# Kernel optimization log

Hardware: AMD Instinct MI355X
Metric: run time of the kernel (lower is better)

## Reference

```python
import jax, jax.numpy as jnp
import numpy as np

N, M, D = 16384, 16384, 256

def setup_inputs() -> dict:
    key = jax.random.key(0)
    kx, ky, kp = jax.random.split(key, 3)
    x = jax.random.normal(kx, (N, D), dtype=jnp.float32)
    y = jax.random.normal(ky, (M, D), dtype=jnp.float32)
    psi = jax.random.normal(kp, (M,), dtype=jnp.float32)
    return {"x": x, "y": y, "psi": psi}

def reference(x, y, psi):
    # cxy[i,j] = ||x_i||^2 + ||y_j||^2 - 2 <x_i, y_j>   (squared euclidean)
    x2 = jnp.sum(x * x, axis=1, keepdims=True)          # [N,1]
    y2 = jnp.sum(y * y, axis=1)[None, :]                # [1,M]
    cxy = x2 + y2 - 2.0 * (x @ y.T)                     # [N,M]
    psi_conjugate_mean = jnp.mean(jnp.min(cxy - psi[None, :], axis=1))
    psi_mean = jnp.mean(psi)
    return (psi_conjugate_mean, psi_mean)
```

## Files before the change

kernel.cpp:

```cpp
#include <hip/hip_runtime.h>
#include <hip/hip_bf16.h>
#include <hip/hip_fp8.h>

#define N_ROWS 16384
#define M_ROWS 16384
#define DIM 256
#define JT 64
#define NJ 32

typedef __attribute__((ext_vector_type(4))) float f32x4;
typedef __attribute__((ext_vector_type(4))) int   i32x4;
typedef __attribute__((ext_vector_type(8))) int   i32x8;

__device__ inline unsigned enc_f(float f) {
  unsigned u = __float_as_uint(f);
  return (u & 0x80000000u) ? ~u : (u | 0x80000000u);
}
__device__ inline float dec_f(unsigned u) {
  unsigned b = (u & 0x80000000u) ? (u & 0x7FFFFFFFu) : ~u;
  return __uint_as_float(b);
}

__global__ __launch_bounds__(256) void prep_kernel(
    const float* __restrict__ x, const float* __restrict__ y,
    const float* __restrict__ psi,
    unsigned char* __restrict__ xb8, unsigned char* __restrict__ yb8,
    float* __restrict__ x2, float* __restrict__ rj,
    unsigned int* __restrict__ rowmin) {
  int bid  = blockIdx.x;
  int isY  = bid >= (N_ROWS / 4);
  int rb   = isY ? bid - N_ROWS / 4 : bid;
  int row  = rb * 4 + (threadIdx.x >> 6);
  int lane = threadIdx.x & 63;
  const float* in = isY ? y : x;
  unsigned char* outb = isY ? yb8 : xb8;
  const float4 v = *reinterpret_cast<const float4*>(in + (size_t)row * DIM + lane * 4);
  unsigned b0 = __hip_fp8_e4m3(v.x).__x;
  unsigned b1 = __hip_fp8_e4m3(v.y).__x;
  unsigned b2 = __hip_fp8_e4m3(v.z).__x;
  unsigned b3 = __hip_fp8_e4m3(v.w).__x;
  *reinterpret_cast<unsigned int*>(outb + (size_t)row * DIM + lane * 4) =
      b0 | (b1 << 8) | (b2 << 16) | (b3 << 24);
  float s = v.x * v.x + v.y * v.y + v.z * v.z + v.w * v.w;
#pragma unroll
  for (int m = 1; m < 64; m <<= 1) s += __shfl_xor(s, m, 64);
  if (lane == 0) {
    if (isY) rj[row] = s - psi[row];
    else { x2[row] = s; rowmin[row] = 0xFFFFFFFFu; }
  }
}

__global__ __launch_bounds__(256, 2) void gemm_min_kernel(
    const unsigned char* __restrict__ xb8, const unsigned char* __restrict__ yb8,
    const float* __restrict__ rj, unsigned int* __restrict__ rowmin) {
  __shared__ unsigned char Bt[3][JT * DIM];

  const int bid    = blockIdx.x;
  const int jchunk = bid & 7;
  const int strip  = bid >> 3;
  const int brow   = strip * 256;
  const int jbase0 = jchunk * (JT * NJ);

  const int tid = threadIdx.x;
  const int w = tid >> 6, lane = tid & 63;
  const int fr = lane & 15, g4 = lane >> 4;

  const int SC1 = 0x7F7F7F7F;

  i32x8 afr[4][2];
  {
    const unsigned char* aBase = xb8 + (size_t)(brow + w * 64 + fr) * DIM + g4 * 32;
#pragma unroll
    for (int m = 0; m < 4; ++m)
#pragma unroll
      for (int kq = 0; kq < 2; ++kq) {
        afr[m][kq] = *reinterpret_cast<const i32x8*>(aBase + (size_t)(m * 16) * DIM + kq * 128);
        asm volatile("" : "+a"(afr[m][kq]));
      }
  }
  __builtin_amdgcn_sched_barrier(0);

  const int sr16 = lane & 15;
  const int sk32 = (lane >> 4) * 32;

#define STAGE(buf, j)                                                            \
  {                                                                              \
    _Pragma("unroll")                                                            \
    for (int c = 0; c < 4; ++c) {                                                \
      const int p = w * 4 + c;                                                   \
      const int cc = p >> 1, h = p & 1;                                          \
      __builtin_amdgcn_global_load_lds(                                          \
          (const __attribute__((address_space(1))) void*)(                       \
              yb8 + (size_t)(jbase0 + (j) * JT + (cc >> 1) * 16 + sr16) * DIM +  \
              (cc & 1) * 128 + sk32 + h * 16),                                   \
          (__attribute__((address_space(3))) void*)(&Bt[(buf)][cc * 2048 + h * 1024]), \
          16, 0, 0);                                                             \
    }                                                                            \
  }

#define LOADF(dst, NG, KQ)                                                       \
  {                                                                              \
    const int cc = (NG) * 2 + (KQ);                                              \
    i32x4 lo = *reinterpret_cast<const i32x4*>(&B[cc * 2048 + lane * 16]);       \
    i32x4 hi = *reinterpret_cast<const i32x4*>(&B[cc * 2048 + 1024 + lane * 16]); \
    dst[0] = lo[0]; dst[1] = lo[1]; dst[2] = lo[2]; dst[3] = lo[3];              \
    dst[4] = hi[0]; dst[5] = hi[1]; dst[6] = hi[2]; dst[7] = hi[3];              \
  }

#define MFMA4(KQ, NG, PB)                                                        \
  {                                                                              \
    _Pragma("unroll")                                                            \
    for (int m = 0; m < 4; ++m)                                                  \
      acc[m][(NG)] = __builtin_amdgcn_mfma_scale_f32_16x16x128_f8f6f4(           \
          afr[m][(KQ)], PB, acc[m][(NG)], 0, 0, 0, SC1, 0, SC1);                 \
  }

#define SGB_DS_MFMA                                                              \
  __builtin_amdgcn_sched_group_barrier(0x100, 2, 0);                             \
  __builtin_amdgcn_sched_group_barrier(0x008, 4, 0);

  STAGE(0, 0);
  STAGE(1, 1);

  const float* rjc = rj + jbase0;
  float mn[4][4];
#pragma unroll
  for (int m = 0; m < 4; ++m)
#pragma unroll
    for (int r = 0; r < 4; ++r) mn[m][r] = 3.4e38f;

  int rb = 0;
#pragma unroll 1
  for (int j = 0; j < NJ; ++j) {
    if (j == NJ - 1) { asm volatile("s_waitcnt vmcnt(0)" ::: "memory"); }
    else             { asm volatile("s_waitcnt vmcnt(4)" ::: "memory"); }
    __builtin_amdgcn_sched_barrier(0);
    __builtin_amdgcn_s_barrier();
    __builtin_amdgcn_sched_barrier(0);

    float rv[4];
#pragma unroll
    for (int n = 0; n < 4; ++n) rv[n] = rjc[j * JT + n * 16 + fr];
    __builtin_amdgcn_sched_barrier(0);
    if (j + 2 < NJ) {
      int sb = rb + 2; if (sb >= 3) sb -= 3;
      STAGE(sb, j + 2);
    }
    __builtin_amdgcn_sched_barrier(0);

    f32x4 acc[4][4];
#pragma unroll
    for (int m = 0; m < 4; ++m)
#pragma unroll
      for (int n = 0; n < 4; ++n) acc[m][n] = (f32x4){0.f, 0.f, 0.f, 0.f};

    const unsigned char* B = &Bt[rb][0];
    i32x8 pbA, pbB;
    LOADF(pbA, 0, 0);

    __builtin_amdgcn_s_setprio(1);
    __builtin_amdgcn_sched_barrier(0);
    LOADF(pbB, 1, 0); MFMA4(0, 0, pbA); SGB_DS_MFMA;
    LOADF(pbA, 2, 0); MFMA4(0, 1, pbB); SGB_DS_MFMA;
    LOADF(pbB, 3, 0); MFMA4(0, 2, pbA); SGB_DS_MFMA;
    LOADF(pbA, 0, 1); MFMA4(0, 3, pbB); SGB_DS_MFMA;
    LOADF(pbB, 1, 1); MFMA4(1, 0, pbA); SGB_DS_MFMA;
    LOADF(pbA, 2, 1); MFMA4(1, 1, pbB); SGB_DS_MFMA;
    LOADF(pbB, 3, 1); MFMA4(1, 2, pbA); SGB_DS_MFMA;
    MFMA4(1, 3, pbB);
    __builtin_amdgcn_sched_group_barrier(0x008, 4, 0);
    __builtin_amdgcn_sched_barrier(0);
    __builtin_amdgcn_s_setprio(0);

#pragma unroll
    for (int m = 0; m < 4; ++m)
#pragma unroll
      for (int n = 0; n < 4; ++n)
#pragma unroll
        for (int r = 0; r < 4; ++r)
          mn[m][r] = fminf(mn[m][r], fmaf(-2.f, acc[m][n][r], rv[n]));
    rb = rb + 1; if (rb >= 3) rb -= 3;
  }
#undef SGB_DS_MFMA
#undef MFMA4
#undef LOADF
#undef STAGE

#pragma unroll
  for (int m = 0; m < 4; ++m)
#pragma unroll
    for (int r = 0; r < 4; ++r) {
      float v = mn[m][r];
#pragma unroll
      for (int s = 1; s < 16; s <<= 1) v = fminf(v, __shfl_xor(v, s, 64));
      if (fr == 0) {
        int row = brow + w * 64 + m * 16 + g4 * 4 + r;
        atomicMin(&rowmin[row], enc_f(v));
      }
    }
}

__global__ __launch_bounds__(256) void finish1_kernel(
    const float* __restrict__ x2, const unsigned int* __restrict__ rowmin,
    const float* __restrict__ psi, double* __restrict__ partials) {
  int tid = threadIdx.x;
  int i = blockIdx.x * 256 + tid;
  double s0 = (double)x2[i] + (double)dec_f(rowmin[i]);
  double s1 = (double)psi[i];
  __shared__ double sm0[4], sm1[4];
#pragma unroll
  for (int m = 1; m < 64; m <<= 1) { s0 += __shfl_xor(s0, m, 64); s1 += __shfl_xor(s1, m, 64); }
  if ((tid & 63) == 0) { sm0[tid >> 6] = s0; sm1[tid >> 6] = s1; }
  __syncthreads();
  if (tid == 0) {
    partials[blockIdx.x]      = sm0[0] + sm0[1] + sm0[2] + sm0[3];
    partials[64 + blockIdx.x] = sm1[0] + sm1[1] + sm1[2] + sm1[3];
  }
}

__global__ __launch_bounds__(64) void finish2_kernel(
    const double* __restrict__ partials, float* __restrict__ out) {
  int lane = threadIdx.x;
  double s0 = partials[lane];
  double s1 = partials[64 + lane];
#pragma unroll
  for (int m = 1; m < 64; m <<= 1) { s0 += __shfl_xor(s0, m, 64); s1 += __shfl_xor(s1, m, 64); }
  if (lane == 0) {
    out[0] = (float)(s0 / (double)N_ROWS);
    out[1] = (float)(s1 / (double)M_ROWS);
  }
}

extern "C" void kernel_launch(void* const* d_in, const int* in_sizes, int n_in,
                              void* d_out, int out_size, void* d_ws, size_t ws_size,
                              hipStream_t stream) {
  const float* x   = (const float*)d_in[0];
  const float* y   = (const float*)d_in[1];
  const float* psi = (const float*)d_in[2];
  float* out = (float*)d_out;

  char* ws = (char*)d_ws;
  unsigned char* xb8 = (unsigned char*)ws;
  unsigned char* yb8 = (unsigned char*)(ws + (size_t)N_ROWS * DIM);
  float* x2 = (float*)(ws + (size_t)(N_ROWS + M_ROWS) * DIM);
  float* rj = x2 + N_ROWS;
  unsigned int* rowmin = (unsigned int*)(rj + M_ROWS);
  double* partials = (double*)(rowmin + N_ROWS);

  prep_kernel<<<(N_ROWS + M_ROWS) / 4, 256, 0, stream>>>(x, y, psi, xb8, yb8, x2, rj, rowmin);
  gemm_min_kernel<<<(N_ROWS / 256) * 8, 256, 0, stream>>>(xb8, yb8, rj, rowmin);
  finish1_kernel<<<N_ROWS / 256, 256, 0, stream>>>(x2, rowmin, psi, partials);
  finish2_kernel<<<1, 64, 0, stream>>>(partials, out);
}
```

Baseline: 78.09 us.

## Double-buffer accumulators and fold the previous tile's max under current MFMAs

Splits the accumulator into two ping-pong sets so the min/fold epilogue of tile j-1 runs interleaved with the MFMAs of tile j, using sched_group_barrier to place VALU ops between matrix instructions. It also rewrites min(rv - 2*acc) as -2*max(acc - rv/2) by seeding the accumulators with -rv/2, which removes the per-element FMA and leaves only a max. The aim is to hide the VALU epilogue behind MFMA latency, at the cost of doubling accumulator registers (32 extra f32x4), which may lower occupancy or cause spills.

```diff
diff --git a/kernel.cpp b/kernel.cpp
--- a/kernel.cpp
+++ b/kernel.cpp
@@ -107,81 +107,99 @@
     dst[4] = hi[0]; dst[5] = hi[1]; dst[6] = hi[2]; dst[7] = hi[3];              \
   }
 
-#define MFMA4(KQ, NG, PB)                                                        \
+#define MFMA4(AC, KQ, NG, PB)                                                    \
   {                                                                              \
     _Pragma("unroll")                                                            \
     for (int m = 0; m < 4; ++m)                                                  \
-      acc[m][(NG)] = __builtin_amdgcn_mfma_scale_f32_16x16x128_f8f6f4(           \
-          afr[m][(KQ)], PB, acc[m][(NG)], 0, 0, 0, SC1, 0, SC1);                 \
-  }
-
-#define SGB_DS_MFMA                                                              \
+      AC[m][(NG)] = __builtin_amdgcn_mfma_scale_f32_16x16x128_f8f6f4(            \
+          afr[m][(KQ)], PB, AC[m][(NG)], 0, 0, 0, SC1, 0, SC1);                  \
+  }
+
+#define INIT16(AC, NG)                                                           \
+  {                                                                              \
+    _Pragma("unroll")                                                            \
+    for (int m = 0; m < 4; ++m)                                                  \
+      AC[m][(NG)] = (f32x4){nh[(NG)], nh[(NG)], nh[(NG)], nh[(NG)]};             \
+  }
+
+#define FOLD8(AP, G)                                                             \
+  {                                                                              \
+    _Pragma("unroll")                                                            \
+    for (int np = 0; np < 2; ++np)                                               \
+      _Pragma("unroll")                                                          \
+      for (int r = 0; r < 4; ++r)                                                \
+        mx[(G) >> 1][r] = fmaxf(mx[(G) >> 1][r],                                 \
+                                AP[(G) >> 1][((G) & 1) * 2 + np][r]);            \
+  }
+
+#define SGB_G                                                                    \
   __builtin_amdgcn_sched_group_barrier(0x100, 2, 0);                             \
-  __builtin_amdgcn_sched_group_barrier(0x008, 4, 0);
+  __builtin_amdgcn_sched_group_barrier(0x008, 4, 0);                             \
+  __builtin_amdgcn_sched_group_barrier(0x002, 24, 0);
+
+#define ITER(J, AC, AP)                                                          \
+  {                                                                              \
+    if ((J) == NJ - 1) { asm volatile("s_waitcnt vmcnt(0)" ::: "memory"); }      \
+    else               { asm volatile("s_waitcnt vmcnt(4)" ::: "memory"); }      \
+    __builtin_amdgcn_sched_barrier(0);                                           \
+    __builtin_amdgcn_s_barrier();                                                \
+    __builtin_amdgcn_sched_barrier(0);                                           \
+    float rv[4], nh[4];                                                          \
+    _Pragma("unroll")                                                            \
+    for (int n = 0; n < 4; ++n) rv[n] = rjc[(J) * JT + n * 16 + fr];             \
+    __builtin_amdgcn_sched_barrier(0);                                           \
+    if ((J) + 2 < NJ) { int sb = rb + 2; if (sb >= 3) sb -= 3; STAGE(sb, (J) + 2); } \
+    __builtin_amdgcn_sched_barrier(0);                                           \
+    _Pragma("unroll")                                                            \
+    for (int n = 0; n < 4; ++n) nh[n] = -0.5f * rv[n];                           \
+    const unsigned char* B = &Bt[rb][0];                                         \
+    i32x8 pbA, pbB;                                                              \
+    LOADF(pbA, 0, 0);                                                            \
+    __builtin_amdgcn_s_setprio(1);                                               \
+    __builtin_amdgcn_sched_barrier(0);                                           \
+    INIT16(AC, 0);                                                               \
+    LOADF(pbB, 1, 0); MFMA4(AC, 0, 0, pbA); INIT16(AC, 1); FOLD8(AP, 0); SGB_G;  \
+    LOADF(pbA, 2, 0); MFMA4(AC, 0, 1, pbB); INIT16(AC, 2); FOLD8(AP, 1); SGB_G;  \
+    LOADF(pbB, 3, 0); MFMA4(AC, 0, 2, pbA); INIT16(AC, 3); FOLD8(AP, 2); SGB_G;  \
+    LOADF(pbA, 0, 1); MFMA4(AC, 0, 3, pbB); FOLD8(AP, 3); SGB_G;                 \
+    LOADF(pbB, 1, 1); MFMA4(AC, 1, 0, pbA); FOLD8(AP, 4); SGB_G;                 \
+    LOADF(pbA, 2, 1); MFMA4(AC, 1, 1, pbB); FOLD8(AP, 5); SGB_G;                 \
+    LOADF(pbB, 3, 1); MFMA4(AC, 1, 2, pbA); FOLD8(AP, 6); SGB_G;                 \
+    MFMA4(AC, 1, 3, pbB); FOLD8(AP, 7);                                          \
+    __builtin_amdgcn_sched_group_barrier(0x008, 4, 0);                           \
+    __builtin_amdgcn_sched_group_barrier(0x002, 24, 0);                          \
+    __builtin_amdgcn_sched_barrier(0);                                           \
+    __builtin_amdgcn_s_setprio(0);                                               \
+    rb = rb + 1; if (rb >= 3) rb -= 3;                                           \
+  }
 
   STAGE(0, 0);
   STAGE(1, 1);
 
   const float* rjc = rj + jbase0;
-  float mn[4][4];
+  float mx[4][4];
+  f32x4 accA[4][4], accB[4][4];
 #pragma unroll
   for (int m = 0; m < 4; ++m)
 #pragma unroll
-    for (int r = 0; r < 4; ++r) mn[m][r] = 3.4e38f;
+    for (int r = 0; r < 4; ++r) mx[m][r] = -3.4e38f;
+#pragma unroll
+  for (int m = 0; m < 4; ++m)
+#pragma unroll
+    for (int n = 0; n < 4; ++n) accB[m][n] = (f32x4){-3.4e38f, -3.4e38f, -3.4e38f, -3.4e38f};
 
   int rb = 0;
 #pragma unroll 1
-  for (int j = 0; j < NJ; ++j) {
-    if (j == NJ - 1) { asm volatile("s_waitcnt vmcnt(0)" ::: "memory"); }
-    else             { asm volatile("s_waitcnt vmcnt(4)" ::: "memory"); }
-    __builtin_amdgcn_sched_barrier(0);
-    __builtin_amdgcn_s_barrier();
-    __builtin_amdgcn_sched_barrier(0);
-
-    float rv[4];
-#pragma unroll
-    for (int n = 0; n < 4; ++n) rv[n] = rjc[j * JT + n * 16 + fr];
-    __builtin_amdgcn_sched_barrier(0);
-    if (j + 2 < NJ) {
-      int sb = rb + 2; if (sb >= 3) sb -= 3;
-      STAGE(sb, j + 2);
-    }
-    __builtin_amdgcn_sched_barrier(0);
-
-    f32x4 acc[4][4];
-#pragma unroll
-    for (int m = 0; m < 4; ++m)
-#pragma unroll
-      for (int n = 0; n < 4; ++n) acc[m][n] = (f32x4){0.f, 0.f, 0.f, 0.f};
-
-    const unsigned char* B = &Bt[rb][0];
-    i32x8 pbA, pbB;
-    LOADF(pbA, 0, 0);
-
-    __builtin_amdgcn_s_setprio(1);
-    __builtin_amdgcn_sched_barrier(0);
-    LOADF(pbB, 1, 0); MFMA4(0, 0, pbA); SGB_DS_MFMA;
-    LOADF(pbA, 2, 0); MFMA4(0, 1, pbB); SGB_DS_MFMA;
-    LOADF(pbB, 3, 0); MFMA4(0, 2, pbA); SGB_DS_MFMA;
-    LOADF(pbA, 0, 1); MFMA4(0, 3, pbB); SGB_DS_MFMA;
-    LOADF(pbB, 1, 1); MFMA4(1, 0, pbA); SGB_DS_MFMA;
-    LOADF(pbA, 2, 1); MFMA4(1, 1, pbB); SGB_DS_MFMA;
-    LOADF(pbB, 3, 1); MFMA4(1, 2, pbA); SGB_DS_MFMA;
-    MFMA4(1, 3, pbB);
-    __builtin_amdgcn_sched_group_barrier(0x008, 4, 0);
-    __builtin_amdgcn_sched_barrier(0);
-    __builtin_amdgcn_s_setprio(0);
-
-#pragma unroll
-    for (int m = 0; m < 4; ++m)
-#pragma unroll
-      for (int n = 0; n < 4; ++n)
-#pragma unroll
-        for (int r = 0; r < 4; ++r)
-          mn[m][r] = fminf(mn[m][r], fmaf(-2.f, acc[m][n][r], rv[n]));
-    rb = rb + 1; if (rb >= 3) rb -= 3;
-  }
-#undef SGB_DS_MFMA
+  for (int jj = 0; jj < NJ; jj += 2) {
+    ITER(jj,     accA, accB);
+    ITER(jj + 1, accB, accA);
+  }
+#pragma unroll
+  for (int g = 0; g < 8; ++g) FOLD8(accB, g);
+#undef ITER
+#undef SGB_G
+#undef FOLD8
+#undef INIT16
 #undef MFMA4
 #undef LOADF
 #undef STAGE
@@ -190,7 +208,7 @@
   for (int m = 0; m < 4; ++m)
 #pragma unroll
     for (int r = 0; r < 4; ++r) {
-      float v = mn[m][r];
+      float v = -2.0f * mx[m][r];
 #pragma unroll
       for (int s = 1; s < 16; s <<= 1) v = fminf(v, __shfl_xor(v, s, 64));
       if (fr == 0) {
```

Result: slower. 191.6 us (+145.3%).

## Fold bias into MFMA accumulator init and interleave max epilogue with MFMAs

Applied to the files above, without the earlier changes.

The accumulator is now seeded with -0.5*rv instead of zero, so the per-element fmaf is dropped and a plain fmax over acc is tracked, with the -2 scale applied once at the end. The init and fold VALU work is interleaved into the MFMA schedule using sched_group_barrier groups, so it hides behind matrix-core latency instead of running as a serial epilogue after each tile. This changes the rounding order slightly, since the bias is now added inside the accumulator.

```diff
diff --git a/kernel.cpp b/kernel.cpp
--- a/kernel.cpp
+++ b/kernel.cpp
@@ -115,19 +115,36 @@
           afr[m][(KQ)], PB, acc[m][(NG)], 0, 0, 0, SC1, 0, SC1);                 \
   }
 
-#define SGB_DS_MFMA                                                              \
+#define INIT16(NG)                                                               \
+  {                                                                              \
+    _Pragma("unroll")                                                            \
+    for (int m = 0; m < 4; ++m)                                                  \
+      acc[m][(NG)] = (f32x4){nh[(NG)], nh[(NG)], nh[(NG)], nh[(NG)]};            \
+  }
+
+#define FOLD16(NG)                                                               \
+  {                                                                              \
+    _Pragma("unroll")                                                            \
+    for (int m = 0; m < 4; ++m)                                                  \
+      _Pragma("unroll")                                                          \
+      for (int r = 0; r < 4; ++r)                                                \
+        mx[m][r] = fmaxf(mx[m][r], acc[m][(NG)][r]);                             \
+  }
+
+#define SGB_G                                                                    \
   __builtin_amdgcn_sched_group_barrier(0x100, 2, 0);                             \
-  __builtin_amdgcn_sched_group_barrier(0x008, 4, 0);
+  __builtin_amdgcn_sched_group_barrier(0x008, 4, 0);                             \
+  __builtin_amdgcn_sched_group_barrier(0x002, 16, 0);
 
   STAGE(0, 0);
   STAGE(1, 1);
 
   const float* rjc = rj + jbase0;
-  float mn[4][4];
+  float mx[4][4];
 #pragma unroll
   for (int m = 0; m < 4; ++m)
 #pragma unroll
-    for (int r = 0; r < 4; ++r) mn[m][r] = 3.4e38f;
+    for (int r = 0; r < 4; ++r) mx[m][r] = -3.4e38f;
 
   int rb = 0;
 #pragma unroll 1
@@ -138,7 +155,7 @@
     __builtin_amdgcn_s_barrier();
     __builtin_amdgcn_sched_barrier(0);
 
-    float rv[4];
+    float rv[4], nh[4];
 #pragma unroll
     for (int n = 0; n < 4; ++n) rv[n] = rjc[j * JT + n * 16 + fr];
     __builtin_amdgcn_sched_barrier(0);
@@ -147,41 +164,36 @@
       STAGE(sb, j + 2);
     }
     __builtin_amdgcn_sched_barrier(0);
+#pragma unroll
+    for (int n = 0; n < 4; ++n) nh[n] = -0.5f * rv[n];
 
     f32x4 acc[4][4];
-#pragma unroll
-    for (int m = 0; m < 4; ++m)
-#pragma unroll
-      for (int n = 0; n < 4; ++n) acc[m][n] = (f32x4){0.f, 0.f, 0.f, 0.f};
-
     const unsigned char* B = &Bt[rb][0];
     i32x8 pbA, pbB;
     LOADF(pbA, 0, 0);
+    INIT16(0);
 
     __builtin_amdgcn_s_setprio(1);
     __builtin_amdgcn_sched_barrier(0);
-    LOADF(pbB, 1, 0); MFMA4(0, 0, pbA); SGB_DS_MFMA;
-    LOADF(pbA, 2, 0); MFMA4(0, 1, pbB); SGB_DS_MFMA;
-    LOADF(pbB, 3, 0); MFMA4(0, 2, pbA); SGB_DS_MFMA;
-    LOADF(pbA, 0, 1); MFMA4(0, 3, pbB); SGB_DS_MFMA;
-    LOADF(pbB, 1, 1); MFMA4(1, 0, pbA); SGB_DS_MFMA;
-    LOADF(pbA, 2, 1); MFMA4(1, 1, pbB); SGB_DS_MFMA;
-    LOADF(pbB, 3, 1); MFMA4(1, 2, pbA); SGB_DS_MFMA;
-    MFMA4(1, 3, pbB);
+    LOADF(pbB, 1, 0); MFMA4(0, 0, pbA); INIT16(1); SGB_G;
+    LOADF(pbA, 2, 0); MFMA4(0, 1, pbB); INIT16(2); SGB_G;
+    LOADF(pbB, 3, 0); MFMA4(0, 2, pbA); INIT16(3); SGB_G;
+    LOADF(pbA, 0, 1); MFMA4(0, 3, pbB); SGB_G;
+    LOADF(pbB, 1, 1); MFMA4(1, 0, pbA); SGB_G;
+    LOADF(pbA, 2, 1); MFMA4(1, 1, pbB); FOLD16(0); SGB_G;
+    LOADF(pbB, 3, 1); MFMA4(1, 2, pbA); FOLD16(1); SGB_G;
+    MFMA4(1, 3, pbB); FOLD16(2);
     __builtin_amdgcn_sched_group_barrier(0x008, 4, 0);
+    __builtin_amdgcn_sched_group_barrier(0x002, 16, 0);
     __builtin_amdgcn_sched_barrier(0);
     __builtin_amdgcn_s_setprio(0);
 
-#pragma unroll
-    for (int m = 0; m < 4; ++m)
-#pragma unroll
-      for (int n = 0; n < 4; ++n)
-#pragma unroll
-        for (int r = 0; r < 4; ++r)
-          mn[m][r] = fminf(mn[m][r], fmaf(-2.f, acc[m][n][r], rv[n]));
+    FOLD16(3);
     rb = rb + 1; if (rb >= 3) rb -= 3;
   }
-#undef SGB_DS_MFMA
+#undef SGB_G
+#undef FOLD16
+#undef INIT16
 #undef MFMA4
 #undef LOADF
 #undef STAGE
@@ -190,7 +202,7 @@
   for (int m = 0; m < 4; ++m)
 #pragma unroll
     for (int r = 0; r < 4; ++r) {
-      float v = mn[m][r];
+      float v = -2.0f * mx[m][r];
 #pragma unroll
       for (int s = 1; s < 16; s <<= 1) v = fminf(v, __shfl_xor(v, s, 64));
       if (fr == 0) {
```

After: 79.22 us. No clear change (+1.4%).
